# Kernel tuning notes

Hardware: AMD Instinct MI355X
Metric: run time of the kernel (lower is better)

## Reference

```python
import jax, jax.numpy as jnp
import numpy as np
import math

WP, WF = 10, 10      # past/future window
EPS = 1e-8           # torch cosine_similarity eps
CLIP = 1.0 - 1e-6    # keep arccos (and its grad) finite
MAXN = 110           # hard-coded alpha width in the module


def setup_inputs() -> dict:
    key = jax.random.key(0)
    k1, k2, k3, k4, k5, k6 = jax.random.split(key, 6)
    B, L, G, N, D = 32, 110, 512, 40, 300
    node_features = jax.random.normal(k1, (B, L, G), jnp.float32)
    knowledge = jax.random.normal(k2, (B, L, N, D), jnp.float32)
    anew = jax.random.uniform(k3, (B, L, N), jnp.float32)
    var_sem = 2.0 / (G + G)
    var_con = 2.0 / (D + D)
    weight_sem = jax.random.normal(k4, (G, G), jnp.float32) * var_sem
    weight_con = jax.random.normal(k5, (D, D), jnp.float32) * var_con
    text_len = jax.random.randint(k6, (B,), 55, L + 1, jnp.int32)
    return dict(node_features=node_features, knowledge=knowledge, anew=anew,
                weight_sem=weight_sem, weight_con=weight_con, text_len=text_len)


def reference(node_features, knowledge, anew, weight_sem, weight_con, text_len):
    B, L, G = node_features.shape
    N = knowledge.shape[2]
    dt = node_features.dtype

    # window + validity mask, replaces per-(i,j) python slicing: [B, j, k]
    j = jnp.arange(L)[:, None]
    k = jnp.arange(L)[None, :]
    cur = text_len[:, None, None]
    mask = (k >= j - WP) & (k <= j + WF)
    mask = mask[None] & (k[None, :, :] <= cur - 1) & (j[None, :, :] < cur)
    fmask = mask.astype(dt)

    # ---- semantic branch: score = 1 - acos(cos_sim(f_j, W_sem f_k))/pi, windowed softmax
    att_sem = jnp.einsum('st,blt->bls', weight_sem, node_features)      # [B,L,G]
    num = jnp.einsum('bjg,bkg->bjk', node_features, att_sem)
    nf = jnp.maximum(jnp.linalg.norm(node_features, axis=-1), EPS)      # [B,L]
    na = jnp.maximum(jnp.linalg.norm(att_sem, axis=-1), EPS)            # [B,L]
    cos = num / (nf[:, :, None] * na[:, None, :])
    score = 1.0 - jnp.arccos(jnp.clip(cos, -CLIP, CLIP)) / math.pi
    neg = jnp.finfo(dt).min
    s = jnp.where(mask, score, neg)
    s = s - jnp.max(s, axis=-1, keepdims=True)
    e = jnp.exp(s) * fmask
    alphas_sem = e / jnp.maximum(jnp.sum(e, axis=-1, keepdims=True), EPS)  # [B,L,L]

    # ---- affinity transform of anew: v -> (||[v, v/2] - [0.5, 0]|| - 0.06467)/0.607468
    anew_aff = (jnp.sqrt((anew - 0.5) ** 2 + (0.5 * anew) ** 2) - 0.06467) / 0.607468

    # ---- contextual branch: windowed sum_n |cos_sim(aff_feat_{k,n}, knowledge_{j,n})|
    att_con = jnp.einsum('blns,st->blnt', knowledge, weight_con)        # [B,L,N,D]
    aff_feat = att_con * anew_aff[..., None]                            # [B,L,N,D]
    num_c = jnp.einsum('bknd,bjnd->bjkn', aff_feat, knowledge)          # [B,j,k,N]
    n_f = jnp.maximum(jnp.linalg.norm(aff_feat, axis=-1), EPS)          # [B,k,N]
    n_k = jnp.maximum(jnp.linalg.norm(knowledge, axis=-1), EPS)         # [B,j,N]
    cos_c = num_c / (n_f[:, None, :, :] * n_k[:, :, None, :])
    alphas_con = 10.0 * jnp.sum(jnp.abs(cos_c), axis=-1) * fmask        # [B,j,k]

    out = 0.5 * alphas_sem + 0.5 * alphas_con                           # [B,L,L]
    if L < MAXN:  # module hard-codes width 110
        out = jnp.pad(out, ((0, 0), (0, 0), (0, MAXN - L)))
    return out
```

## Files before the change

### kernel.cpp

```cpp
#include <hip/hip_runtime.h>
#include <hip/hip_bf16.h>
#include <math.h>

constexpr int Bb   = 32;
constexpr int Ls   = 110;
constexpr int Gs   = 512;
constexpr int Ns   = 40;
constexpr int Ds   = 300;
constexpr int WPc  = 10;
constexpr int WFc  = 10;
constexpr int MAXNc = 110;
constexpr float EPSf  = 1e-8f;
constexpr float CLIPf = 1.0f - 1e-6f;
constexpr int BL = Bb * Ls;
constexpr int Mrows = BL * Ns;
constexpr int BPITCH = 328;
constexpr int KST = 320;
constexpr int RGRP = Mrows / 256;

constexpr int PREP_BLOCKS = 2048;
constexpr int SGEMM_BLOCKS = BL / 8;
constexpr int CGEMM_BLOCKS = 2208;

typedef __attribute__((ext_vector_type(8))) short short8_t;
typedef __attribute__((ext_vector_type(4))) float floatx4;

__device__ __forceinline__ unsigned short bf16r(float f) {
  unsigned u = __float_as_uint(f);
  u += 0x7fffu + ((u >> 16) & 1u);
  return (unsigned short)(u >> 16);
}

__device__ __forceinline__ unsigned pkbf(float lo, float hi) {
  unsigned a = __float_as_uint(lo), b = __float_as_uint(hi);
  a += 0x7fffu + ((a >> 16) & 1u);
  b += 0x7fffu + ((b >> 16) & 1u);
  return (a >> 16) | (b & 0xffff0000u);
}

__device__ __forceinline__ short8_t cvt8(const float4 v0, const float4 v1) {
  union { short8_t s; unsigned u[4]; } p;
  p.u[0] = pkbf(v0.x, v0.y);
  p.u[1] = pkbf(v0.z, v0.w);
  p.u[2] = pkbf(v1.x, v1.y);
  p.u[3] = pkbf(v1.z, v1.w);
  return p.s;
}

__global__ __launch_bounds__(256) void transpose_wsem(const float* __restrict__ w,
                                                      float* __restrict__ wt) {
  __shared__ float tile[32][33];
  const int bx = blockIdx.x * 32;
  const int by = blockIdx.y * 32;
  const int tx = threadIdx.x;
  const int ty = threadIdx.y;
#pragma unroll
  for (int r = ty; r < 32; r += 8)
    tile[r][tx] = w[(by + r) * Gs + (bx + tx)];
  __syncthreads();
#pragma unroll
  for (int r = ty; r < 32; r += 8)
    wt[(bx + r) * Gs + (by + tx)] = tile[tx][r];
}

__global__ __launch_bounds__(256) void wct_prep(const float* __restrict__ wc,
                                                short* __restrict__ wct) {
  __shared__ float tile[32][33];
  const int t0 = blockIdx.x * 32;
  const int s0 = blockIdx.y * 32;
  const int tx = threadIdx.x, ty = threadIdx.y;
#pragma unroll
  for (int r = ty; r < 32; r += 8) {
    const int s = s0 + r, t = t0 + tx;
    tile[r][tx] = (s < Ds && t < Ds) ? wc[s * Ds + t] : 0.f;
  }
  __syncthreads();
#pragma unroll
  for (int r = ty; r < 32; r += 8) {
    const int t = t0 + r, s = s0 + tx;
    wct[t * KST + s] = (short)bf16r(tile[tx][r]);
  }
}

__global__ __launch_bounds__(512) void fused_prep_semgemm(
    const float* __restrict__ kn, unsigned short* __restrict__ knb,
    float* __restrict__ kninv,
    const float* __restrict__ nf, const float* __restrict__ wt,
    float* __restrict__ att_sem, float* __restrict__ na_arr) {
  __shared__ float partial[8][8];

  if (blockIdx.x < PREP_BLOCKS) {
    const int wid = (blockIdx.x * 512 + threadIdx.x) >> 6;
    const int lane = threadIdx.x & 63;
    const int nwaves = PREP_BLOCKS * 8;
    for (int row = wid; row < Mrows; row += nwaves) {
      const float* __restrict__ src = kn + (size_t)row * Ds;
      float4 v0 = make_float4(0.f, 0.f, 0.f, 0.f);
      float4 v1 = v0;
      const int d0 = lane * 8;
      if (lane < 37) {
        v0 = *reinterpret_cast<const float4*>(src + d0);
        v1 = *reinterpret_cast<const float4*>(src + d0 + 4);
      } else if (lane == 37) {
        v0 = *reinterpret_cast<const float4*>(src + d0);
      }
      float ss = v0.x * v0.x + v0.y * v0.y + v0.z * v0.z + v0.w * v0.w +
                 v1.x * v1.x + v1.y * v1.y + v1.z * v1.z + v1.w * v1.w;
#pragma unroll
      for (int off = 32; off > 0; off >>= 1) ss += __shfl_xor(ss, off);
      if (lane < 40)
        *reinterpret_cast<short8_t*>(knb + (size_t)row * KST + d0) = cvt8(v0, v1);
      if (lane == 0) kninv[row] = 1.0f / fmaxf(sqrtf(ss), EPSf);
    }
  } else {
    const int bl0 = (blockIdx.x - PREP_BLOCKS) * 8;
    const int s = threadIdx.x;
    const float* __restrict__ x0 = nf + (size_t)bl0 * Gs;
    float acc[8];
#pragma unroll
    for (int r = 0; r < 8; ++r) acc[r] = 0.f;
#pragma unroll 4
    for (int t = 0; t < Gs; ++t) {
      const float wv = wt[t * Gs + s];
#pragma unroll
      for (int r = 0; r < 8; ++r) acc[r] = fmaf(wv, x0[r * Gs + t], acc[r]);
    }
#pragma unroll
    for (int r = 0; r < 8; ++r) att_sem[(size_t)(bl0 + r) * Gs + s] = acc[r];

    const int wave = s >> 6, lane = s & 63;
#pragma unroll
    for (int r = 0; r < 8; ++r) {
      float v = acc[r] * acc[r];
#pragma unroll
      for (int off = 32; off > 0; off >>= 1) v += __shfl_xor(v, off);
      if (lane == 0) partial[r][wave] = v;
    }
    __syncthreads();
    if (s < 8) {
      float sum = 0.f;
#pragma unroll
      for (int w2 = 0; w2 < 8; ++w2) sum += partial[s][w2];
      na_arr[bl0 + s] = fmaxf(sqrtf(sum), EPSf);
    }
  }
}

__global__ __launch_bounds__(256, 3) void fused_congemm_semattn(
    const unsigned short* __restrict__ knb, const short* __restrict__ wct,
    const int* __restrict__ tlen,
    unsigned short* __restrict__ ybar, float* __restrict__ rowss,
    const float* __restrict__ nf, const float* __restrict__ att_sem,
    const float* __restrict__ na_arr, float* __restrict__ out) {
  __shared__ short Bl[80 * BPITCH];
  __shared__ float sred[4];
  __shared__ float ssc[21];

  if (blockIdx.x < CGEMM_BLOCKS) {
    const int lin = blockIdx.x;
    const int xcd = lin & 7, slot = lin >> 3;
    const int m = slot & 3;
    const int g = xcd + 8 * (slot >> 2);
    if (g >= RGRP) return;
    const int rowbase = g * 256;
    const int n0 = m * 80;

    const int tid = threadIdx.x;
    for (int s = tid; s < 80 * 40; s += 256) {
      const int nl = s / 40, sl = s % 40;
      *reinterpret_cast<short8_t*>(&Bl[nl * BPITCH + sl * 8]) =
          *reinterpret_cast<const short8_t*>(wct + (n0 + nl) * KST + sl * 8);
    }
    __syncthreads();

    const int wave = tid >> 6, lane = tid & 63;
    const int quad = lane >> 4, l16 = lane & 15;
    const int wrow = rowbase + wave * 64;

    {
      bool any = false;
      for (int bl = wrow / Ns; bl <= (wrow + 63) / Ns; ++bl)
        any |= (bl % Ls) < tlen[bl / Ls];
      if (!any) return;
    }

    const unsigned short* arow[4];
#pragma unroll
    for (int tt = 0; tt < 4; ++tt)
      arow[tt] = knb + (size_t)(wrow + tt * 16 + l16) * KST + quad * 8;

    floatx4 acc[4][5];
#pragma unroll
    for (int tt = 0; tt < 4; ++tt)
#pragma unroll
      for (int i = 0; i < 5; ++i) acc[tt][i] = (floatx4){0.f, 0.f, 0.f, 0.f};

    short8_t A[3][4];
#pragma unroll
    for (int tt = 0; tt < 4; ++tt) {
      A[0][tt] = *reinterpret_cast<const short8_t*>(arow[tt]);
      A[1][tt] = *reinterpret_cast<const short8_t*>(arow[tt] + 32);
    }

#pragma unroll
    for (int c = 0; c < 10; ++c) {
      if (c < 8) {
#pragma unroll
        for (int tt = 0; tt < 4; ++tt)
          A[(c + 2) % 3][tt] =
              *reinterpret_cast<const short8_t*>(arow[tt] + (c + 2) * 32);
      }
#pragma unroll
      for (int i = 0; i < 5; ++i) {
        const short8_t bfrag = *reinterpret_cast<const short8_t*>(
            &Bl[(i * 16 + l16) * BPITCH + c * 32 + quad * 8]);
#pragma unroll
        for (int tt = 0; tt < 4; ++tt)
          acc[tt][i] = __builtin_amdgcn_mfma_f32_16x16x32_bf16(
              A[c % 3][tt], bfrag, acc[tt][i], 0, 0, 0);
      }
    }

#pragma unroll
    for (int tt = 0; tt < 4; ++tt) {
      const int row0 = wrow + tt * 16;
      const int blA = row0 / Ns, blB = (row0 + 15) / Ns;
      const bool alive =
          ((blA % Ls) < tlen[blA / Ls]) | ((blB % Ls) < tlen[blB / Ls]);
      if (!alive) continue;

#pragma unroll
      for (int r = 0; r < 4; ++r) {
        float p = 0.f;
#pragma unroll
        for (int i = 0; i < 5; ++i) p = fmaf(acc[tt][i][r], acc[tt][i][r], p);
        p += __shfl_xor(p, 1);
        p += __shfl_xor(p, 2);
        p += __shfl_xor(p, 4);
        p += __shfl_xor(p, 8);
        if (l16 == 0) atomicAdd(&rowss[row0 + quad * 4 + r], p);
      }
#pragma unroll
      for (int i = 0; i < 5; ++i) {
        const int col = n0 + i * 16 + l16;
#pragma unroll
        for (int r = 0; r < 4; ++r)
          ybar[(size_t)(row0 + quad * 4 + r) * KST + col] = bf16r(acc[tt][i][r]);
      }
    }
  } else {
    float* xs = reinterpret_cast<float*>(Bl);
    const int blk = blockIdx.x - CGEMM_BLOCKS;
    const int b = blk / Ls, j = blk % Ls;
    const int len = tlen[b];
    float* __restrict__ orow = out + (size_t)(b * Ls + j) * MAXNc;
    if (j >= len) {
      for (int k = threadIdx.x; k < MAXNc; k += 256) orow[k] = 0.f;
      return;
    }
    const int k0 = max(j - WPc, 0);
    const int k1 = min(j + WFc, len - 1);
    const int nk = k1 - k0 + 1;

    const float* __restrict__ x = nf + (size_t)(b * Ls + j) * Gs;
    float ss = 0.f;
    for (int t = threadIdx.x; t < Gs; t += 256) {
      const float v = x[t];
      xs[t] = v;
      ss += v * v;
    }
    const int wave = threadIdx.x >> 6, lane = threadIdx.x & 63;
#pragma unroll
    for (int off = 32; off > 0; off >>= 1) ss += __shfl_xor(ss, off);
    if (lane == 0) sred[wave] = ss;
    __syncthreads();
    const float nfn = fmaxf(sqrtf(sred[0] + sred[1] + sred[2] + sred[3]), EPSf);

    for (int i = wave; i < nk; i += 4) {
      const int k = k0 + i;
      const float* __restrict__ as = att_sem + (size_t)(b * Ls + k) * Gs;
      float d = 0.f;
#pragma unroll
      for (int t = lane; t < Gs; t += 64) d = fmaf(xs[t], as[t], d);
#pragma unroll
      for (int off = 32; off > 0; off >>= 1) d += __shfl_xor(d, off);
      if (lane == 0) {
        float cs = d / (nfn * na_arr[b * Ls + k]);
        cs = fminf(fmaxf(cs, -CLIPf), CLIPf);
        ssc[i] = 1.0f - acosf(cs) * (float)(1.0 / M_PI);
      }
    }
    __syncthreads();
    if (threadIdx.x == 0) {
      float mx = -1e30f;
      for (int i = 0; i < nk; ++i) mx = fmaxf(mx, ssc[i]);
      sred[0] = mx;
    }
    __syncthreads();
    const float mx = sred[0];
    if ((int)threadIdx.x < nk) ssc[threadIdx.x] = expf(ssc[threadIdx.x] - mx);
    __syncthreads();
    if (threadIdx.x == 0) {
      float s = 0.f;
      for (int i = 0; i < nk; ++i) s += ssc[i];
      sred[1] = 1.0f / fmaxf(s, EPSf);
    }
    __syncthreads();
    const float inv = sred[1];
    for (int k = threadIdx.x; k < MAXNc; k += 256) {
      float v = 0.f;
      if (k >= k0 && k <= k1) v = 0.5f * ssc[k - k0] * inv;
      orow[k] = v;
    }
  }
}

__global__ __launch_bounds__(512) void con_attn_mfma(const unsigned short* __restrict__ knb,
                                                     const unsigned short* __restrict__ ybar,
                                                     const float* __restrict__ rowss,
                                                     const float* __restrict__ kninv,
                                                     const float* __restrict__ anew,
                                                     const int* __restrict__ tlen,
                                                     float* __restrict__ out) {
  const int b = blockIdx.x / 7;
  const int jt = blockIdx.x % 7;
  const int j0 = jt * 16;
  const int len = tlen[b];
  if (j0 >= len) return;
  const int kbase = min(max(j0 - WPc, 0), Ls - 48);

  const int tid = threadIdx.x;
  const int wave = tid >> 6, lane = tid & 63;
  const int quad = lane >> 4, l16 = lane & 15;

  __shared__ float red[8][768];

  const int jj = min(j0 + l16, Ls - 1);
  const size_t blj = (size_t)(b * Ls + jj);

  float outacc[3][4];
#pragma unroll
  for (int t = 0; t < 3; ++t)
#pragma unroll
    for (int r = 0; r < 4; ++r) outacc[t][r] = 0.f;

  const unsigned short* yrow[3];
  int krow_m[3];
#pragma unroll
  for (int t = 0; t < 3; ++t) {
    const int k = kbase + t * 16 + l16;
    yrow[t] = ybar + (size_t)(b * Ls + k) * Ns * KST;
    krow_m[t] = (b * Ls + k) * Ns;
  }

  for (int ni = 0; ni < 5; ++ni) {
    const int n = wave + ni * 8;
    const unsigned short* __restrict__ arow =
        knb + ((blj * Ns + n) * (size_t)KST) + quad * 8;

    float w_t[3];
#pragma unroll
    for (int t = 0; t < 3; ++t) {
      const int mm = krow_m[t] + n;
      const float a = anew[mm];
      const float ssqk = rowss[mm];
      const float aff = (sqrtf((a - 0.5f) * (a - 0.5f) + 0.25f * a * a) - 0.06467f) *
                        (1.0f / 0.607468f);
      w_t[t] = aff / fmaxf(aff * sqrtf(ssqk), EPSf);
    }
    const float kinv = kninv[blj * Ns + n];

    floatx4 S[3];
#pragma unroll
    for (int t = 0; t < 3; ++t) S[t] = (floatx4){0.f, 0.f, 0.f, 0.f};

#pragma unroll
    for (int c = 0; c < 10; ++c) {
      const short8_t afrag = *reinterpret_cast<const short8_t*>(arow + c * 32);
#pragma unroll
      for (int t = 0; t < 3; ++t) {
        const short8_t bfrag = *reinterpret_cast<const short8_t*>(
            yrow[t] + (size_t)n * KST + c * 32 + quad * 8);
        S[t] = __builtin_amdgcn_mfma_f32_16x16x32_bf16(afrag, bfrag, S[t], 0, 0, 0);
      }
    }

#pragma unroll
    for (int r = 0; r < 4; ++r) {
      const float kv = __shfl(kinv, quad * 4 + r);
#pragma unroll
      for (int t = 0; t < 3; ++t)
        outacc[t][r] = fmaf(kv * w_t[t], fabsf(S[t][r]), outacc[t][r]);
    }
  }

#pragma unroll
  for (int t = 0; t < 3; ++t)
#pragma unroll
    for (int r = 0; r < 4; ++r)
      red[wave][(quad * 4 + r) * 48 + t * 16 + l16] = outacc[t][r];
  __syncthreads();

  for (int idx = tid; idx < 768; idx += 512) {
    float s = 0.f;
#pragma unroll
    for (int w = 0; w < 8; ++w) s += red[w][idx];
    const int j = j0 + idx / 48;
    const int k = kbase + idx % 48;
    if (j < len && k < len && k >= j - WPc && k <= j + WFc)
      out[(size_t)(b * Ls + j) * MAXNc + k] += 5.0f * s;
  }
}

extern "C" void kernel_launch(void* const* d_in, const int* in_sizes, int n_in,
                              void* d_out, int out_size, void* d_ws, size_t ws_size,
                              hipStream_t stream) {
  const float* nf   = (const float*)d_in[0];
  const float* kn   = (const float*)d_in[1];
  const float* anew = (const float*)d_in[2];
  const float* wsem = (const float*)d_in[3];
  const float* wcon = (const float*)d_in[4];
  const int*   tlen = (const int*)d_in[5];
  float* out = (float*)d_out;

  float* att_sem = (float*)d_ws;
  float* na_arr  = att_sem + (size_t)BL * Gs;
  float* wt      = na_arr + BL;
  short* wct     = (short*)(wt + (size_t)Gs * Gs);
  float* rowss   = (float*)(wct + KST * KST);
  float* kninv   = rowss + Mrows;
  unsigned short* knb  = (unsigned short*)(kninv + Mrows);
  unsigned short* ybar = knb + (size_t)Mrows * KST;

  hipMemsetAsync(rowss, 0, (size_t)Mrows * sizeof(float), stream);
  transpose_wsem<<<dim3(16, 16), dim3(32, 8), 0, stream>>>(wsem, wt);
  wct_prep<<<dim3(10, 10), dim3(32, 8), 0, stream>>>(wcon, wct);
  fused_prep_semgemm<<<PREP_BLOCKS + SGEMM_BLOCKS, 512, 0, stream>>>(
      kn, knb, kninv, nf, wt, att_sem, na_arr);
  fused_congemm_semattn<<<CGEMM_BLOCKS + BL, 256, 0, stream>>>(
      knb, wct, tlen, ybar, rowss, nf, att_sem, na_arr, out);
  con_attn_mfma<<<Bb * 7, 512, 0, stream>>>(knb, ybar, rowss, kninv, anew, tlen, out);
}
```

Before: 501.1 us.

## Split fused prep/semantic GEMM into separate kernels and register-block sem GEMM

Splits the fused knowledge-prep and semantic-GEMM kernel into two launches. The knowledge prep now uses 256-thread blocks. The semantic GEMM stages its 8 input rows in shared memory and has each thread compute a 2x4 output tile with float4 weight loads, replacing the old one-column-per-thread scheme that read the 8 input rows from global memory. The aim is more reuse of each weight load and fewer redundant global reads, at the cost of one extra launch and no overlap between the two phases.

```diff
diff --git a/kernel.cpp b/kernel.cpp
--- a/kernel.cpp
+++ b/kernel.cpp
@@ -17,9 +17,6 @@
 constexpr int BPITCH = 328;
 constexpr int KST = 320;
 constexpr int RGRP = Mrows / 256;
-
-constexpr int PREP_BLOCKS = 2048;
-constexpr int SGEMM_BLOCKS = BL / 8;
 constexpr int CGEMM_BLOCKS = 2208;
 
 typedef __attribute__((ext_vector_type(8))) short short8_t;
@@ -82,67 +79,95 @@
   }
 }
 
-__global__ __launch_bounds__(512) void fused_prep_semgemm(
-    const float* __restrict__ kn, unsigned short* __restrict__ knb,
-    float* __restrict__ kninv,
-    const float* __restrict__ nf, const float* __restrict__ wt,
-    float* __restrict__ att_sem, float* __restrict__ na_arr) {
-  __shared__ float partial[8][8];
-
-  if (blockIdx.x < PREP_BLOCKS) {
-    const int wid = (blockIdx.x * 512 + threadIdx.x) >> 6;
-    const int lane = threadIdx.x & 63;
-    const int nwaves = PREP_BLOCKS * 8;
-    for (int row = wid; row < Mrows; row += nwaves) {
-      const float* __restrict__ src = kn + (size_t)row * Ds;
-      float4 v0 = make_float4(0.f, 0.f, 0.f, 0.f);
-      float4 v1 = v0;
-      const int d0 = lane * 8;
-      if (lane < 37) {
-        v0 = *reinterpret_cast<const float4*>(src + d0);
-        v1 = *reinterpret_cast<const float4*>(src + d0 + 4);
-      } else if (lane == 37) {
-        v0 = *reinterpret_cast<const float4*>(src + d0);
-      }
-      float ss = v0.x * v0.x + v0.y * v0.y + v0.z * v0.z + v0.w * v0.w +
-                 v1.x * v1.x + v1.y * v1.y + v1.z * v1.z + v1.w * v1.w;
-#pragma unroll
-      for (int off = 32; off > 0; off >>= 1) ss += __shfl_xor(ss, off);
-      if (lane < 40)
-        *reinterpret_cast<short8_t*>(knb + (size_t)row * KST + d0) = cvt8(v0, v1);
-      if (lane == 0) kninv[row] = 1.0f / fmaxf(sqrtf(ss), EPSf);
-    }
-  } else {
-    const int bl0 = (blockIdx.x - PREP_BLOCKS) * 8;
-    const int s = threadIdx.x;
+__global__ __launch_bounds__(256) void kn_prep(const float* __restrict__ kn,
+                                               unsigned short* __restrict__ knb,
+                                               float* __restrict__ kninv) {
+  const int wid = (blockIdx.x * 256 + threadIdx.x) >> 6;
+  const int lane = threadIdx.x & 63;
+  const int nwaves = gridDim.x * 4;
+  for (int row = wid; row < Mrows; row += nwaves) {
+    const float* __restrict__ src = kn + (size_t)row * Ds;
+    float4 v0 = make_float4(0.f, 0.f, 0.f, 0.f);
+    float4 v1 = v0;
+    const int d0 = lane * 8;
+    if (lane < 37) {
+      v0 = *reinterpret_cast<const float4*>(src + d0);
+      v1 = *reinterpret_cast<const float4*>(src + d0 + 4);
+    } else if (lane == 37) {
+      v0 = *reinterpret_cast<const float4*>(src + d0);
+    }
+    float ss = v0.x * v0.x + v0.y * v0.y + v0.z * v0.z + v0.w * v0.w +
+               v1.x * v1.x + v1.y * v1.y + v1.z * v1.z + v1.w * v1.w;
+#pragma unroll
+    for (int off = 32; off > 0; off >>= 1) ss += __shfl_xor(ss, off);
+    if (lane < 40)
+      *reinterpret_cast<short8_t*>(knb + (size_t)row * KST + d0) = cvt8(v0, v1);
+    if (lane == 0) kninv[row] = 1.0f / fmaxf(sqrtf(ss), EPSf);
+  }
+}
+
+__global__ __launch_bounds__(512) void sem_gemm(const float* __restrict__ nf,
+                                                const float* __restrict__ wt,
+                                                float* __restrict__ att_sem,
+                                                float* __restrict__ na_arr) {
+  __shared__ float xs[8][Gs];
+  __shared__ float red[4][2][2];
+  const int bl0 = blockIdx.x * 8;
+  const int tid = threadIdx.x;
+
+  {
     const float* __restrict__ x0 = nf + (size_t)bl0 * Gs;
-    float acc[8];
-#pragma unroll
-    for (int r = 0; r < 8; ++r) acc[r] = 0.f;
-#pragma unroll 4
-    for (int t = 0; t < Gs; ++t) {
-      const float wv = wt[t * Gs + s];
-#pragma unroll
-      for (int r = 0; r < 8; ++r) acc[r] = fmaf(wv, x0[r * Gs + t], acc[r]);
-    }
-#pragma unroll
-    for (int r = 0; r < 8; ++r) att_sem[(size_t)(bl0 + r) * Gs + s] = acc[r];
-
-    const int wave = s >> 6, lane = s & 63;
-#pragma unroll
-    for (int r = 0; r < 8; ++r) {
-      float v = acc[r] * acc[r];
-#pragma unroll
-      for (int off = 32; off > 0; off >>= 1) v += __shfl_xor(v, off);
-      if (lane == 0) partial[r][wave] = v;
-    }
-    __syncthreads();
-    if (s < 8) {
-      float sum = 0.f;
-#pragma unroll
-      for (int w2 = 0; w2 < 8; ++w2) sum += partial[s][w2];
-      na_arr[bl0 + s] = fmaxf(sqrtf(sum), EPSf);
-    }
+    const int base = tid * 8;
+    const float4 a = *reinterpret_cast<const float4*>(x0 + base);
+    const float4 b = *reinterpret_cast<const float4*>(x0 + base + 4);
+    *reinterpret_cast<float4*>(&xs[0][0] + base) = a;
+    *reinterpret_cast<float4*>(&xs[0][0] + base + 4) = b;
+  }
+  __syncthreads();
+
+  const int sq = tid & 127;
+  const int g  = tid >> 7;
+  float4 acc0 = make_float4(0.f, 0.f, 0.f, 0.f);
+  float4 acc1 = make_float4(0.f, 0.f, 0.f, 0.f);
+  const float* __restrict__ wp = wt + sq * 4;
+  const float* __restrict__ xa = &xs[2 * g][0];
+  const float* __restrict__ xb = &xs[2 * g + 1][0];
+
+#pragma unroll 8
+  for (int t = 0; t < Gs; ++t) {
+    const float4 wv = *reinterpret_cast<const float4*>(wp + (size_t)t * Gs);
+    const float va = xa[t];
+    const float vb = xb[t];
+    acc0.x = fmaf(wv.x, va, acc0.x);
+    acc0.y = fmaf(wv.y, va, acc0.y);
+    acc0.z = fmaf(wv.z, va, acc0.z);
+    acc0.w = fmaf(wv.w, va, acc0.w);
+    acc1.x = fmaf(wv.x, vb, acc1.x);
+    acc1.y = fmaf(wv.y, vb, acc1.y);
+    acc1.z = fmaf(wv.z, vb, acc1.z);
+    acc1.w = fmaf(wv.w, vb, acc1.w);
+  }
+
+  *reinterpret_cast<float4*>(&att_sem[(size_t)(bl0 + 2 * g) * Gs + sq * 4]) = acc0;
+  *reinterpret_cast<float4*>(&att_sem[(size_t)(bl0 + 2 * g + 1) * Gs + sq * 4]) = acc1;
+
+  float s0 = acc0.x * acc0.x + acc0.y * acc0.y + acc0.z * acc0.z + acc0.w * acc0.w;
+  float s1 = acc1.x * acc1.x + acc1.y * acc1.y + acc1.z * acc1.z + acc1.w * acc1.w;
+#pragma unroll
+  for (int off = 32; off > 0; off >>= 1) {
+    s0 += __shfl_xor(s0, off);
+    s1 += __shfl_xor(s1, off);
+  }
+  const int half = (tid >> 6) & 1;
+  if ((tid & 63) == 0) {
+    red[g][half][0] = s0;
+    red[g][half][1] = s1;
+  }
+  __syncthreads();
+  if (tid < 8) {
+    const int gg = tid >> 1, rr = tid & 1;
+    const float sum = red[gg][0][rr] + red[gg][1][rr];
+    na_arr[bl0 + 2 * gg + rr] = fmaxf(sqrtf(sum), EPSf);
   }
 }
 
@@ -435,8 +460,8 @@
   hipMemsetAsync(rowss, 0, (size_t)Mrows * sizeof(float), stream);
   transpose_wsem<<<dim3(16, 16), dim3(32, 8), 0, stream>>>(wsem, wt);
   wct_prep<<<dim3(10, 10), dim3(32, 8), 0, stream>>>(wcon, wct);
-  fused_prep_semgemm<<<PREP_BLOCKS + SGEMM_BLOCKS, 512, 0, stream>>>(
-      kn, knb, kninv, nf, wt, att_sem, na_arr);
+  kn_prep<<<2048, 256, 0, stream>>>(kn, knb, kninv);
+  sem_gemm<<<BL / 8, 512, 0, stream>>>(nf, wt, att_sem, na_arr);
   fused_congemm_semattn<<<CGEMM_BLOCKS + BL, 256, 0, stream>>>(
       knb, wct, tlen, ybar, rowss, nf, att_sem, na_arr, out);
   con_attn_mfma<<<Bb * 7, 512, 0, stream>>>(knb, ybar, rowss, kninv, anew, tlen, out);
```

Result: faster. 484.7 us (-3.3%).
